# Kernel tuning notes

Hardware: AMD Instinct MI355X
Metric: run time of the kernel (lower is better)

The kernel has to match this reference:

```python
import jax, jax.numpy as jnp
import numpy as np

N_SAMPLES = 5        # samples_per_num
N_ITERS = 10         # n_iter_sinkhorn
TEMP = 1.0
NOISE_FACTOR = 1.0
EPS = 1e-20

def setup_inputs() -> dict:
    key = jax.random.key(0)
    ks = jax.random.split(key, 6)
    B, n, latent = 512, 128, 128
    x = jax.random.normal(ks[0], (B, n), dtype=jnp.float32)
    w1 = jax.random.normal(ks[1], (latent, 1), dtype=jnp.float32) * (1.0)
    b1 = jax.random.normal(ks[2], (latent,), dtype=jnp.float32) * 0.1
    w2 = jax.random.normal(ks[3], (n, latent), dtype=jnp.float32) * (1.0 / np.sqrt(latent))
    b2 = jax.random.normal(ks[4], (n,), dtype=jnp.float32) * 0.1
    # Gumbel(0,1) noise for samples_per_num * B matrices
    u = jax.random.uniform(ks[5], (N_SAMPLES * B, n, n), dtype=jnp.float32)
    noise = -jnp.log(-jnp.log(u + EPS) + EPS)
    return {"x": x, "w1": w1, "b1": b1, "w2": w2, "b2": b2, "noise": noise}

def reference(x, w1, b1, w2, b2, noise):
    B, n = x.shape
    # per-scalar MLP: [B*n, 1] -> [B*n, latent] -> [B*n, n]
    h = jax.nn.relu(x.reshape(-1, 1) @ w1.T + b1)
    log_alpha = (h @ w2.T + b2).reshape(B, n, n)
    # tile across samples, add gumbel noise, divide by temperature
    la = jnp.tile(log_alpha, (N_SAMPLES, 1, 1))          # [S*B, n, n]
    la = (la + noise * NOISE_FACTOR) / TEMP
    # Sinkhorn: alternating row/column logsumexp normalization in log space
    def step(la, _):
        la = la - jax.scipy.special.logsumexp(la, axis=2, keepdims=True)
        la = la - jax.scipy.special.logsumexp(la, axis=1, keepdims=True)
        return la, None
    la, _ = jax.lax.scan(step, la, None, length=N_ITERS)
    # soft_perms_inf: exp, view [S,B,n,n], transpose(0,1) -> [B,S,n,n]
    # inv_soft_pers_flattened: transpose last two dims, transpose(0,1) back, flatten
    inv = jnp.exp(la).reshape(N_SAMPLES, B, n, n).transpose(0, 1, 3, 2)
    return inv.reshape(-1, n, n)                          # [S*B, n, n]
```

## Files before the change

kernel.cpp:

```cpp
#include <hip/hip_runtime.h>

#define NN   128
#define NB   512
#define NMAT 2560
#define L2E  1.4426950408889634f

typedef __attribute__((ext_vector_type(4))) float  f32x4;
typedef __attribute__((ext_vector_type(4))) int    i32x4;
typedef __attribute__((ext_vector_type(8))) ushort u16x8;

__device__ __forceinline__ float fexp2(float x){ float r; asm("v_exp_f32 %0, %1" : "=v"(r) : "v"(x)); return r; }
__device__ __forceinline__ float flog2(float x){ float r; asm("v_log_f32 %0, %1" : "=v"(r) : "v"(x)); return r; }
__device__ __forceinline__ float frcp (float x){ float r; asm("v_rcp_f32 %0, %1" : "=v"(r) : "v"(x)); return r; }

__device__ __forceinline__ ushort f2bf(float f){
    unsigned u = __float_as_uint(f);
    unsigned r = (u + 0x7FFFu + ((u >> 16) & 1u)) >> 16;
    return (ushort)r;
}
__device__ __forceinline__ float bf2f(ushort h){ return __uint_as_float(((unsigned)h) << 16); }

#define MFMA16(acc, a, b) \
    asm("v_mfma_f32_16x16x32_bf16 %0, %1, %2, %0" : "+v"(acc) : "v"(a), "v"(b))

__global__ __launch_bounds__(256) void prep_kernel(
    const float* __restrict__ w2, const float* __restrict__ b2,
    ushort* __restrict__ Bhi, ushort* __restrict__ Blo, float* __restrict__ b2s)
{
    int fid = blockIdx.x * 256 + threadIdx.x;
    int ct = fid >> 8, ks = (fid >> 6) & 3, lane = fid & 63;
    int c  = ct * 16 + (lane & 15);
    int k0 = ks * 32 + ((lane >> 4) << 3);
    u16x8 hi, lo;
#pragma unroll
    for (int j = 0; j < 8; j++) {
        float v = w2[c * NN + k0 + j] * L2E;
        ushort h = f2bf(v);
        hi[j] = h;
        lo[j] = f2bf(v - bf2f(h));
    }
    *(u16x8*)(Bhi + (size_t)fid * 8) = hi;
    *(u16x8*)(Blo + (size_t)fid * 8) = lo;
    if (fid < NN) b2s[fid] = b2[fid] * L2E;
}

__global__ __launch_bounds__(256) void mlp_mfma_kernel(
    const float* __restrict__ x,  const float* __restrict__ w1,
    const float* __restrict__ b1, const ushort* __restrict__ Bhi,
    const ushort* __restrict__ Blo, const float* __restrict__ b2s,
    float* __restrict__ la)
{
    const int t    = threadIdx.x;
    const int w    = t >> 6;
    const int lane = t & 63;
    const int blk  = blockIdx.x;
    const int b    = blk >> 1;
    const int rh   = blk & 1;

    const int r = rh * 64 + w * 16 + (lane & 15);
    const float xv = x[b * NN + r];

    i32x4 Ahi[4], Alo[4];
#pragma unroll
    for (int ks = 0; ks < 4; ks++) {
        const int l0 = ks * 32 + ((lane >> 4) << 3);
        float4 w1a = *(const float4*)(w1 + l0);
        float4 w1b = *(const float4*)(w1 + l0 + 4);
        float4 b1a = *(const float4*)(b1 + l0);
        float4 b1b = *(const float4*)(b1 + l0 + 4);
        float h[8];
        h[0] = fmaxf(fmaf(xv, w1a.x, b1a.x), 0.f);
        h[1] = fmaxf(fmaf(xv, w1a.y, b1a.y), 0.f);
        h[2] = fmaxf(fmaf(xv, w1a.z, b1a.z), 0.f);
        h[3] = fmaxf(fmaf(xv, w1a.w, b1a.w), 0.f);
        h[4] = fmaxf(fmaf(xv, w1b.x, b1b.x), 0.f);
        h[5] = fmaxf(fmaf(xv, w1b.y, b1b.y), 0.f);
        h[6] = fmaxf(fmaf(xv, w1b.z, b1b.z), 0.f);
        h[7] = fmaxf(fmaf(xv, w1b.w, b1b.w), 0.f);
#pragma unroll
        for (int p = 0; p < 4; p++) {
            ushort h0 = f2bf(h[2 * p]);
            ushort h1 = f2bf(h[2 * p + 1]);
            ushort l0e = f2bf(h[2 * p]     - bf2f(h0));
            ushort l1e = f2bf(h[2 * p + 1] - bf2f(h1));
            ((int*)&Ahi[ks])[p] = ((int)h1 << 16) | (int)h0;
            ((int*)&Alo[ks])[p] = ((int)l1e << 16) | (int)l0e;
        }
    }

    f32x4 acc[8];
#pragma unroll
    for (int ct = 0; ct < 8; ct++) acc[ct] = (f32x4){0.f, 0.f, 0.f, 0.f};

    asm volatile("s_nop 7");

#pragma unroll
    for (int ks = 0; ks < 4; ks++) {
#pragma unroll
        for (int ct = 0; ct < 8; ct++) {
            const size_t off = ((size_t)(ct * 4 + ks) * 64 + lane) * 8;
            i32x4 bh = *(const i32x4*)(Bhi + off);
            i32x4 bl = *(const i32x4*)(Blo + off);
            MFMA16(acc[ct], Ahi[ks], bh);
            MFMA16(acc[ct], Ahi[ks], bl);
            MFMA16(acc[ct], Alo[ks], bh);
        }
    }

    asm volatile("s_nop 7");
    asm volatile("s_nop 7");
    asm volatile("s_nop 3");

    const int row0 = b * NN + rh * 64 + w * 16 + (lane >> 4) * 4;
    const int col  = lane & 15;
#pragma unroll
    for (int ct = 0; ct < 8; ct++) {
        float bb = b2s[ct * 16 + col];
        float* lp = la + (size_t)row0 * NN + ct * 16 + col;
#pragma unroll
        for (int q = 0; q < 4; q++)
            lp[(size_t)q * NN] = acc[ct][q] + bb;
    }
}

__global__ __launch_bounds__(512, 6) void sinkhorn_kernel(
    const float* __restrict__ la, const float* __restrict__ noise,
    float* __restrict__ out)
{
    __shared__ float part[32][132];
    __shared__ float tbuf[128];

    const int m  = blockIdx.x;
    const int b  = m & (NB - 1);
    const int t  = threadIdx.x;
    const int tr = t >> 4, tc = t & 15;
    const int r0 = tr * 4, c0 = tc * 8;

    const float* lab = la    + (size_t)b * NN * NN;
    const float* nb  = noise + (size_t)m * NN * NN;

    float E[4][8];
#pragma unroll
    for (int i = 0; i < 4; i++) {
        const float* lr = lab + (r0 + i) * NN + c0;
        const float* nr = nb  + (r0 + i) * NN + c0;
        float4 a0 = *(const float4*)(lr);
        float4 a1 = *(const float4*)(lr + 4);
        float4 n0 = *(const float4*)(nr);
        float4 n1 = *(const float4*)(nr + 4);
        E[i][0] = fmaf(n0.x, L2E, a0.x);
        E[i][1] = fmaf(n0.y, L2E, a0.y);
        E[i][2] = fmaf(n0.z, L2E, a0.z);
        E[i][3] = fmaf(n0.w, L2E, a0.w);
        E[i][4] = fmaf(n1.x, L2E, a1.x);
        E[i][5] = fmaf(n1.y, L2E, a1.y);
        E[i][6] = fmaf(n1.z, L2E, a1.z);
        E[i][7] = fmaf(n1.w, L2E, a1.w);
    }

#pragma unroll
    for (int i = 0; i < 4; i++) {
        float mx = E[i][0];
#pragma unroll
        for (int j = 1; j < 8; j++) mx = fmaxf(mx, E[i][j]);
#pragma unroll
        for (int s = 1; s < 16; s <<= 1) mx = fmaxf(mx, __shfl_xor(mx, s));
        float sm = 0.f;
#pragma unroll
        for (int j = 0; j < 8; j++) sm += fexp2(E[i][j] - mx);
#pragma unroll
        for (int s = 1; s < 16; s <<= 1) sm += __shfl_xor(sm, s);
        float R1 = mx + flog2(sm);
#pragma unroll
        for (int j = 0; j < 8; j++) E[i][j] = fexp2(E[i][j] - R1);
    }

    float u[4];
#pragma unroll
    for (int i = 0; i < 4; i++) u[i] = 1.f;
    float tj[8];

    for (int k = 0; k < 10; k++) {
        float loc[8];
#pragma unroll
        for (int j = 0; j < 8; j++) {
            float s = 0.f;
#pragma unroll
            for (int i = 0; i < 4; i++) s = fmaf(E[i][j], u[i], s);
            loc[j] = s;
        }
        *(float4*)&part[tr][c0]     = make_float4(loc[0], loc[1], loc[2], loc[3]);
        *(float4*)&part[tr][c0 + 4] = make_float4(loc[4], loc[5], loc[6], loc[7]);
        __syncthreads();
        {
            const int col = t >> 2;
            const int q   = t & 3;
            float cs = 0.f;
#pragma unroll
            for (int p = 0; p < 8; p++) cs += part[q + 4 * p][col];
            cs += __shfl_xor(cs, 1);
            cs += __shfl_xor(cs, 2);
            if (q == 0) tbuf[col] = frcp(cs);
        }
        __syncthreads();
        {
            float4 t0 = *(const float4*)&tbuf[c0];
            float4 t1 = *(const float4*)&tbuf[c0 + 4];
            tj[0] = t0.x; tj[1] = t0.y; tj[2] = t0.z; tj[3] = t0.w;
            tj[4] = t1.x; tj[5] = t1.y; tj[6] = t1.z; tj[7] = t1.w;
        }
        if (k < 9) {
#pragma unroll
            for (int i = 0; i < 4; i++) {
                float s = 0.f;
#pragma unroll
                for (int j = 0; j < 8; j++) s = fmaf(E[i][j], tj[j], s);
#pragma unroll
                for (int sf = 1; sf < 16; sf <<= 1) s += __shfl_xor(s, sf);
                u[i] = frcp(s);
            }
        }
    }

    float* ob = out + (size_t)m * NN * NN;
#pragma unroll
    for (int j = 0; j < 8; j++) {
        float4 v;
        v.x = E[0][j] * u[0] * tj[j];
        v.y = E[1][j] * u[1] * tj[j];
        v.z = E[2][j] * u[2] * tj[j];
        v.w = E[3][j] * u[3] * tj[j];
        *(float4*)(ob + (c0 + j) * NN + r0) = v;
    }
}

extern "C" void kernel_launch(void* const* d_in, const int* in_sizes, int n_in,
                              void* d_out, int out_size, void* d_ws, size_t ws_size,
                              hipStream_t stream) {
    const float* x     = (const float*)d_in[0];
    const float* w1    = (const float*)d_in[1];
    const float* b1    = (const float*)d_in[2];
    const float* w2    = (const float*)d_in[3];
    const float* b2    = (const float*)d_in[4];
    const float* noise = (const float*)d_in[5];
    float* out = (float*)d_out;

    char* ws  = (char*)d_ws;
    float*  la  = (float*)ws;
    ushort* Bhi = (ushort*)(ws + 33554432);
    ushort* Blo = (ushort*)(ws + 33554432 + 32768);
    float*  b2s = (float*)(ws + 33554432 + 65536);

    hipLaunchKernelGGL(prep_kernel, dim3(8), dim3(256), 0, stream,
                       w2, b2, Bhi, Blo, b2s);
    hipLaunchKernelGGL(mlp_mfma_kernel, dim3(1024), dim3(256), 0, stream,
                       x, w1, b1, Bhi, Blo, b2s, la);
    hipLaunchKernelGGL(sinkhorn_kernel, dim3(NMAT), dim3(512), 0, stream,
                       la, noise, out);
}
```

Measured before the change: 132.4 us.

## Keep transposed copy of E in registers to replace column reduction with shuffles

After the initial row normalization, each thread also holds a transposed 4x8 tile of E, built through a two-pass shared-memory transpose. The column sums in the Sinkhorn loop then become wave-level shuffle reductions instead of a shared-memory partial-sum reduction. The row and column scale vectors are exchanged through small shared buffers, and the final output is written row-contiguous from the transposed tile. This doubles register use for E, so the occupancy hint drops from 6 to 5 blocks, and it adds a one-time transpose with extra barriers.

```diff
diff --git a/kernel.cpp b/kernel.cpp
--- a/kernel.cpp
+++ b/kernel.cpp
@@ -123,12 +123,13 @@
     }
 }
 
-__global__ __launch_bounds__(512, 6) void sinkhorn_kernel(
+__global__ __launch_bounds__(512, 5) void sinkhorn_kernel(
     const float* __restrict__ la, const float* __restrict__ noise,
     float* __restrict__ out)
 {
-    __shared__ float part[32][132];
+    __shared__ float buf[64][133];
     __shared__ float tbuf[128];
+    __shared__ float ubuf[128];
 
     const int m  = blockIdx.x;
     const int b  = m & (NB - 1);
@@ -175,41 +176,71 @@
         for (int j = 0; j < 8; j++) E[i][j] = fexp2(E[i][j] - R1);
     }
 
-    float u[4];
-#pragma unroll
-    for (int i = 0; i < 4; i++) u[i] = 1.f;
-    float tj[8];
+    float F[8][4];
+    if (tr < 16) {
+#pragma unroll
+        for (int i = 0; i < 4; i++) {
+            *(float4*)&buf[r0 + i][c0]     = make_float4(E[i][0], E[i][1], E[i][2], E[i][3]);
+            *(float4*)&buf[r0 + i][c0 + 4] = make_float4(E[i][4], E[i][5], E[i][6], E[i][7]);
+        }
+    }
+    __syncthreads();
+    if (tc < 8) {
+#pragma unroll
+        for (int j = 0; j < 8; j++) {
+            float4 v = *(const float4*)&buf[c0 + j][r0];
+            F[j][0] = v.x; F[j][1] = v.y; F[j][2] = v.z; F[j][3] = v.w;
+        }
+    }
+    __syncthreads();
+    if (tr >= 16) {
+#pragma unroll
+        for (int i = 0; i < 4; i++) {
+            *(float4*)&buf[r0 - 64 + i][c0]     = make_float4(E[i][0], E[i][1], E[i][2], E[i][3]);
+            *(float4*)&buf[r0 - 64 + i][c0 + 4] = make_float4(E[i][4], E[i][5], E[i][6], E[i][7]);
+        }
+    }
+    __syncthreads();
+    if (tc >= 8) {
+#pragma unroll
+        for (int j = 0; j < 8; j++) {
+            float4 v = *(const float4*)&buf[c0 - 64 + j][r0];
+            F[j][0] = v.x; F[j][1] = v.y; F[j][2] = v.z; F[j][3] = v.w;
+        }
+    }
+
+    float uj[8], ti[4];
 
     for (int k = 0; k < 10; k++) {
-        float loc[8];
-#pragma unroll
-        for (int j = 0; j < 8; j++) {
+        if (k > 0) {
+            float4 u0 = *(const float4*)&ubuf[c0];
+            float4 u1 = *(const float4*)&ubuf[c0 + 4];
+            uj[0] = u0.x; uj[1] = u0.y; uj[2] = u0.z; uj[3] = u0.w;
+            uj[4] = u1.x; uj[5] = u1.y; uj[6] = u1.z; uj[7] = u1.w;
+        } else {
+#pragma unroll
+            for (int j = 0; j < 8; j++) uj[j] = 1.f;
+        }
+#pragma unroll
+        for (int i = 0; i < 4; i++) {
             float s = 0.f;
 #pragma unroll
-            for (int i = 0; i < 4; i++) s = fmaf(E[i][j], u[i], s);
-            loc[j] = s;
-        }
-        *(float4*)&part[tr][c0]     = make_float4(loc[0], loc[1], loc[2], loc[3]);
-        *(float4*)&part[tr][c0 + 4] = make_float4(loc[4], loc[5], loc[6], loc[7]);
+            for (int j = 0; j < 8; j++) s = fmaf(F[j][i], uj[j], s);
+#pragma unroll
+            for (int sf = 1; sf < 16; sf <<= 1) s += __shfl_xor(s, sf);
+            ti[i] = frcp(s);
+        }
+        if (tc == 0)
+            *(float4*)&tbuf[r0] = make_float4(ti[0], ti[1], ti[2], ti[3]);
         __syncthreads();
-        {
-            const int col = t >> 2;
-            const int q   = t & 3;
-            float cs = 0.f;
-#pragma unroll
-            for (int p = 0; p < 8; p++) cs += part[q + 4 * p][col];
-            cs += __shfl_xor(cs, 1);
-            cs += __shfl_xor(cs, 2);
-            if (q == 0) tbuf[col] = frcp(cs);
-        }
-        __syncthreads();
-        {
+
+        if (k < 9) {
+            float tj[8];
             float4 t0 = *(const float4*)&tbuf[c0];
             float4 t1 = *(const float4*)&tbuf[c0 + 4];
             tj[0] = t0.x; tj[1] = t0.y; tj[2] = t0.z; tj[3] = t0.w;
             tj[4] = t1.x; tj[5] = t1.y; tj[6] = t1.z; tj[7] = t1.w;
-        }
-        if (k < 9) {
+            float uo[4];
 #pragma unroll
             for (int i = 0; i < 4; i++) {
                 float s = 0.f;
@@ -217,20 +248,28 @@
                 for (int j = 0; j < 8; j++) s = fmaf(E[i][j], tj[j], s);
 #pragma unroll
                 for (int sf = 1; sf < 16; sf <<= 1) s += __shfl_xor(s, sf);
-                u[i] = frcp(s);
+                uo[i] = frcp(s);
             }
-        }
-    }
-
-    float* ob = out + (size_t)m * NN * NN;
-#pragma unroll
-    for (int j = 0; j < 8; j++) {
-        float4 v;
-        v.x = E[0][j] * u[0] * tj[j];
-        v.y = E[1][j] * u[1] * tj[j];
-        v.z = E[2][j] * u[2] * tj[j];
-        v.w = E[3][j] * u[3] * tj[j];
-        *(float4*)(ob + (c0 + j) * NN + r0) = v;
+            if (tc == 0)
+                *(float4*)&ubuf[r0] = make_float4(uo[0], uo[1], uo[2], uo[3]);
+            __syncthreads();
+        } else {
+            float* ob = out + (size_t)m * NN * NN;
+#pragma unroll
+            for (int i = 0; i < 4; i++) {
+                float4 v0, v1;
+                v0.x = F[0][i] * uj[0] * ti[i];
+                v0.y = F[1][i] * uj[1] * ti[i];
+                v0.z = F[2][i] * uj[2] * ti[i];
+                v0.w = F[3][i] * uj[3] * ti[i];
+                v1.x = F[4][i] * uj[4] * ti[i];
+                v1.y = F[5][i] * uj[5] * ti[i];
+                v1.z = F[6][i] * uj[6] * ti[i];
+                v1.w = F[7][i] * uj[7] * ti[i];
+                *(float4*)(ob + (size_t)(r0 + i) * NN + c0)     = v0;
+                *(float4*)(ob + (size_t)(r0 + i) * NN + c0 + 4) = v1;
+            }
+        }
     }
 }
 
```

After: 214.6 us. 1.62x slower.
